# Kernel tuning notes

Measured on AMD Instinct MI355X. Metric: run time of the kernel, lower is better.

## Reference

```python
import jax, jax.numpy as jnp
import numpy as np

SIZE_A, SIZE_B = 5, 5
C, B, H, W = 20, 2, 64, 2048


def _gauss_depthwise_kernel(size_a, size_b, num_classes, sq_var):
    # per-class 2D gaussian with zeroed center; shape (C, 1, ka, kb) for depthwise OIHW
    ii = (np.arange(size_a) - size_a // 2).astype(np.float32)
    jj = (np.arange(size_b) - size_b // 2).astype(np.float32)
    d2 = ii[:, None] ** 2 + jj[None, :] ** 2  # (ka, kb)
    sv = np.asarray(sq_var, dtype=np.float32)[:, None, None]  # (C,1,1)
    k = np.exp(-d2[None] / (2.0 * sv))  # (C, ka, kb)
    k[:, size_a // 2, size_b // 2] = 0.0
    return jnp.asarray(k[:, None], dtype=jnp.float32)


def _depthwise_conv(x, w):
    pa, pb = w.shape[2] // 2, w.shape[3] // 2
    return jax.lax.conv_general_dilated(
        x, w, window_strides=(1, 1), padding=((pa, pa), (pb, pb)),
        dimension_numbers=("NCHW", "OIHW", "NCHW"),
        feature_group_count=x.shape[1])


def setup_inputs() -> dict:
    key = jax.random.key(0)
    k1, k2, k3 = jax.random.split(key, 3)
    sq_var_ang = np.ones(C, dtype=np.float32)
    sq_var_bi = sq_var_ang  # sq_var_bi=None -> defaults to sq_var_ang
    return {
        "data": jax.random.normal(k1, (B, C, H, W), dtype=jnp.float32),
        "mask": jax.random.uniform(k2, (B, 1, H, W), dtype=jnp.float32),
        "bilateral": jax.random.uniform(k3, (B, 1, SIZE_A * SIZE_B - 1, H, W), dtype=jnp.float32),
        "ang_w": _gauss_depthwise_kernel(SIZE_A, SIZE_B, C, sq_var_ang),
        "bi_w": _gauss_depthwise_kernel(SIZE_A, SIZE_B, C, sq_var_bi),
    }


def reference(data, mask, bilateral, ang_w, bi_w):
    b, c, h, w = data.shape
    ka, kb = ang_w.shape[2], ang_w.shape[3]
    pa, pb = ka // 2, kb // 2
    K = ka * kb - 1

    # ang_conv / bi_ang_conv: dense CxC conv whose kernel is diagonal == depthwise gaussian conv
    ang = _depthwise_conv(data, ang_w)
    bi_ang = _depthwise_conv(data, bi_w)

    # condense_conv: one-hot kernels == neighbor extraction of masked data (zero-padded),
    # channel order (neighbor, class) exactly as the torch kernel layout, center removed.
    xm = data * mask
    xp = jnp.pad(xm, ((0, 0), (0, 0), (pa, pa), (pb, pb)))
    neigh = [xp[:, :, i:i + h, j:j + w]
             for i in range(ka) for j in range(kb)
             if not (i == pa and j == pb)]
    cond = jnp.stack(neigh, axis=1)  # (b, K, c, h, w) -- row-major flat order (neighbor, class)
    # torch .view(b, c, -1, h, w) reinterprets the (K*c) channel axis row-major as (c, K):
    cond = cond.reshape(b, c, K, h, w)

    bi_out = (cond * bilateral).sum(axis=2) * mask * bi_ang
    return ang, bi_out
```

## Files before the change

kernel.cpp:

```cpp
#include <hip/hip_runtime.h>

#define C_     20
#define H_     64
#define W_     2048
#define HW_    (H_*W_)
#define KN     24
#define TH     8
#define TW     64
#define TR     (TH+4)
#define TC     (TW+4)
#define PLANE  (TR*TC)
#define DELEMS (C_*PLANE)
#define DPAD   16384
#define NTHR   512
#define DSTG   (DPAD/NTHR)
#define MPAD   1024

#define GLOAD_LDS(SRC, DST)                                                     \
    __builtin_amdgcn_global_load_lds(                                           \
        (const __attribute__((address_space(1))) void*)(SRC),                   \
        (__attribute__((address_space(3))) void*)(DST), 4, 0, 0)

constexpr int KI[KN] = {0,0,0,0,0, 1,1,1,1,1, 2,2,2,2, 3,3,3,3,3, 4,4,4,4,4};
constexpr int KJ[KN] = {0,1,2,3,4, 0,1,2,3,4, 0,1,3,4, 0,1,2,3,4, 0,1,2,3,4};

__global__ __launch_bounds__(NTHR, 4) void lp_kernel(
    const float* __restrict__ data,
    const float* __restrict__ mask,
    const float* __restrict__ bilat,
    const float* __restrict__ ang_w,
    const float* __restrict__ bi_w,
    const float* __restrict__ zbuf,
    float* __restrict__ out)
{
    __shared__ float s_data[DPAD];
    __shared__ float s_mask[MPAD];

    const int tid = threadIdx.x;
    int bid = blockIdx.x;
    bid = (bid & 7)*64 + (bid >> 3);

    const int tx = bid & 31;
    const int ty = (bid >> 5) & 7;
    const int b  = bid >> 8;
    const int y0 = ty*TH, x0 = tx*TW;

    const float* dbase = data + (size_t)b*C_*HW_;
    const float* mbase = mask + (size_t)b*HW_;
    const int wbase = tid & ~63;

#pragma unroll
    for (int s = 0; s < DSTG; ++s) {
        const int idx = tid + s*NTHR;
        const int cls = idx / PLANE;
        const int rem = idx - cls*PLANE;
        const int r   = rem / TC;
        const int col = rem - r*TC;
        const int gy = y0 + r - 2, gx = x0 + col - 2;
        const bool ok = (idx < DELEMS) & (gy >= 0) & (gy < H_) & (gx >= 0) & (gx < W_);
        const float* src = ok ? (dbase + (size_t)cls*HW_ + (gy*W_ + gx)) : zbuf;
        GLOAD_LDS(src, s_data + s*NTHR + wbase);
    }
#pragma unroll
    for (int s = 0; s < MPAD/NTHR; ++s) {
        const int idx = tid + s*NTHR;
        const int r   = idx / TC;
        const int col = idx - r*TC;
        const int gy = y0 + r - 2, gx = x0 + col - 2;
        const bool ok = (idx < PLANE) & (gy >= 0) & (gy < H_) & (gx >= 0) & (gx < W_);
        const float* src = ok ? (mbase + (gy*W_ + gx)) : zbuf;
        GLOAD_LDS(src, s_mask + s*NTHR + wbase);
    }

    const int lx  = tid & 63;
    const int lyy = tid >> 6;
    const int y = y0 + lyy, x = x0 + lx;

    float bb[KN];
    {
        const float* bibase = bilat + (size_t)b*KN*HW_ + (size_t)y*W_ + x;
#pragma unroll
        for (int kp = 0; kp < KN; ++kp) bb[kp] = bibase[(size_t)kp*HW_];
    }

    __syncthreads();

    float mm[KN];
#pragma unroll
    for (int k = 0; k < KN; ++k) mm[k] = s_mask[(lyy + KI[k])*TC + (lx + KJ[k])];
    const float m_c = s_mask[(lyy + 2)*TC + (lx + 2)];

    float bi_acc[C_], biang[C_];
#pragma unroll
    for (int c2 = 0; c2 < C_; ++c2) bi_acc[c2] = 0.0f;

    float* aout = out + ((size_t)b*C_*H_ + y)*W_ + x;
    float* bout = aout + (size_t)2*C_*HW_;

#pragma unroll
    for (int cls = 0; cls < C_; ++cls) {
        float a = 0.0f, ba = 0.0f;
        const float* srow = s_data + cls*PLANE + lyy*TC + lx;
#pragma unroll
        for (int k = 0; k < KN; ++k) {
            const int i = KI[k], j = KJ[k];
            const float v = srow[i*TC + j];
            a  += ang_w[cls*25 + i*5 + j] * v;
            ba += bi_w [cls*25 + i*5 + j] * v;
            const int flat = k*C_ + cls;
            bi_acc[flat / KN] += bb[flat % KN] * (v * mm[k]);
        }
        aout[(size_t)cls*HW_] = a;
        biang[cls] = ba;
    }

#pragma unroll
    for (int c2 = 0; c2 < C_; ++c2)
        bout[(size_t)c2*HW_] = m_c * biang[c2] * bi_acc[c2];
}

extern "C" void kernel_launch(void* const* d_in, const int* in_sizes, int n_in,
                              void* d_out, int out_size, void* d_ws, size_t ws_size,
                              hipStream_t stream) {
    const float* data  = (const float*)d_in[0];
    const float* mask  = (const float*)d_in[1];
    const float* bilat = (const float*)d_in[2];
    const float* ang_w = (const float*)d_in[3];
    const float* bi_w  = (const float*)d_in[4];
    float* out = (float*)d_out;

    hipMemsetAsync(d_ws, 0, 256, stream);

    const int nblocks = 2 * (H_/TH) * (W_/TW);
    lp_kernel<<<nblocks, NTHR, 0, stream>>>(data, mask, bilat, ang_w, bi_w,
                                            (const float*)d_ws, out);
}
```

Before: 33.55 us.

## Transpose shared data tile to class-innermost layout and loop neighbors outermost

The data tile in LDS is stored as position-major with 21-float padded class stride instead of class planes, loaded through registers rather than direct global-to-LDS loads. The compute loop is reordered to iterate neighbors outermost and read all 20 classes contiguously per neighbor, keeping a, ba and bi accumulators in registers. This is meant to cut LDS address computation and enable wider LDS reads. In exchange it raises register pressure (60 accumulators plus 24 bilateral values), and the LDS writes from the strided transpose may bank-conflict.

```diff
diff --git a/kernel.cpp b/kernel.cpp
--- a/kernel.cpp
+++ b/kernel.cpp
@@ -11,9 +11,9 @@
 #define TC     (TW+4)
 #define PLANE  (TR*TC)
 #define DELEMS (C_*PLANE)
-#define DPAD   16384
 #define NTHR   512
-#define DSTG   (DPAD/NTHR)
+#define DSTG   32
+#define SCLS   21
 #define MPAD   1024
 
 #define GLOAD_LDS(SRC, DST)                                                     \
@@ -33,7 +33,7 @@
     const float* __restrict__ zbuf,
     float* __restrict__ out)
 {
-    __shared__ float s_data[DPAD];
+    __shared__ float s_data[PLANE*SCLS];
     __shared__ float s_mask[MPAD];
 
     const int tid = threadIdx.x;
@@ -49,18 +49,17 @@
     const float* mbase = mask + (size_t)b*HW_;
     const int wbase = tid & ~63;
 
+    const int lx  = tid & 63;
+    const int lyy = tid >> 6;
+    const int y = y0 + lyy, x = x0 + lx;
+
+    float bb[KN];
+    {
+        const float* bibase = bilat + (size_t)b*KN*HW_ + (size_t)y*W_ + x;
 #pragma unroll
-    for (int s = 0; s < DSTG; ++s) {
-        const int idx = tid + s*NTHR;
-        const int cls = idx / PLANE;
-        const int rem = idx - cls*PLANE;
-        const int r   = rem / TC;
-        const int col = rem - r*TC;
-        const int gy = y0 + r - 2, gx = x0 + col - 2;
-        const bool ok = (idx < DELEMS) & (gy >= 0) & (gy < H_) & (gx >= 0) & (gx < W_);
-        const float* src = ok ? (dbase + (size_t)cls*HW_ + (gy*W_ + gx)) : zbuf;
-        GLOAD_LDS(src, s_data + s*NTHR + wbase);
+        for (int kp = 0; kp < KN; ++kp) bb[kp] = bibase[(size_t)kp*HW_];
     }
+
 #pragma unroll
     for (int s = 0; s < MPAD/NTHR; ++s) {
         const int idx = tid + s*NTHR;
@@ -72,51 +71,57 @@
         GLOAD_LDS(src, s_mask + s*NTHR + wbase);
     }
 
-    const int lx  = tid & 63;
-    const int lyy = tid >> 6;
-    const int y = y0 + lyy, x = x0 + lx;
+#pragma unroll
+    for (int s = 0; s < DSTG; ++s) {
+        const int g = tid + s*NTHR;
+        if (g < DELEMS) {
+            const int cls = g / PLANE;
+            const int pos = g - cls*PLANE;
+            const int r   = pos / TC;
+            const int col = pos - r*TC;
+            const int gy = y0 + r - 2, gx = x0 + col - 2;
+            const bool ok = (gy >= 0) & (gy < H_) & (gx >= 0) & (gx < W_);
+            const float* src = ok ? (dbase + (size_t)cls*HW_ + (gy*W_ + gx)) : dbase;
+            float v = *src;
+            s_data[pos*SCLS + cls] = ok ? v : 0.0f;
+        }
+    }
+    __syncthreads();
 
-    float bb[KN];
-    {
-        const float* bibase = bilat + (size_t)b*KN*HW_ + (size_t)y*W_ + x;
+    float a[C_], ba[C_], bi[C_];
 #pragma unroll
-        for (int kp = 0; kp < KN; ++kp) bb[kp] = bibase[(size_t)kp*HW_];
+    for (int c = 0; c < C_; ++c) { a[c] = 0.0f; ba[c] = 0.0f; bi[c] = 0.0f; }
+
+    const float* sbase = s_data + (lyy*TC + lx)*SCLS;
+    const int    mbase_l = lyy*TC + lx;
+
+#pragma unroll
+    for (int k = 0; k < KN; ++k) {
+        const int i = KI[k], j = KJ[k];
+        const float mm_k = s_mask[mbase_l + i*TC + j];
+        const float* p = sbase + (i*TC + j)*SCLS;
+        float v[C_];
+#pragma unroll
+        for (int c = 0; c < C_; ++c) v[c] = p[c];
+#pragma unroll
+        for (int c = 0; c < C_; ++c) {
+            a[c]  = fmaf(ang_w[c*25 + i*5 + j], v[c], a[c]);
+            ba[c] = fmaf(bi_w [c*25 + i*5 + j], v[c], ba[c]);
+            const int flat = k*C_ + c;
+            bi[flat/KN] = fmaf(bb[flat%KN], v[c]*mm_k, bi[flat/KN]);
+        }
     }
 
-    __syncthreads();
-
-    float mm[KN];
-#pragma unroll
-    for (int k = 0; k < KN; ++k) mm[k] = s_mask[(lyy + KI[k])*TC + (lx + KJ[k])];
-    const float m_c = s_mask[(lyy + 2)*TC + (lx + 2)];
-
-    float bi_acc[C_], biang[C_];
-#pragma unroll
-    for (int c2 = 0; c2 < C_; ++c2) bi_acc[c2] = 0.0f;
+    const float m_c = s_mask[mbase_l + 2*TC + 2];
 
     float* aout = out + ((size_t)b*C_*H_ + y)*W_ + x;
     float* bout = aout + (size_t)2*C_*HW_;
 
 #pragma unroll
-    for (int cls = 0; cls < C_; ++cls) {
-        float a = 0.0f, ba = 0.0f;
-        const float* srow = s_data + cls*PLANE + lyy*TC + lx;
-#pragma unroll
-        for (int k = 0; k < KN; ++k) {
-            const int i = KI[k], j = KJ[k];
-            const float v = srow[i*TC + j];
-            a  += ang_w[cls*25 + i*5 + j] * v;
-            ba += bi_w [cls*25 + i*5 + j] * v;
-            const int flat = k*C_ + cls;
-            bi_acc[flat / KN] += bb[flat % KN] * (v * mm[k]);
-        }
-        aout[(size_t)cls*HW_] = a;
-        biang[cls] = ba;
+    for (int c = 0; c < C_; ++c) {
+        aout[(size_t)c*HW_] = a[c];
+        bout[(size_t)c*HW_] = m_c * ba[c] * bi[c];
     }
-
-#pragma unroll
-    for (int c2 = 0; c2 < C_; ++c2)
-        bout[(size_t)c2*HW_] = m_c * biang[c2] * bi_acc[c2];
 }
 
 extern "C" void kernel_launch(void* const* d_in, const int* in_sizes, int n_in,
```

Result: slower. 101.3 us (+201.8%).

## Split class staging into two LDS chunks to overlap loads with compute

Applied to the files above, without the earlier changes.

The 20-class data tile is now staged into LDS as two halves of 10 classes in separate buffers. The second half's global-to-LDS loads are issued after the first barrier, so they can run while the first half is being convolved. A second barrier waits for them before the second half is computed. This targets the stall where every thread waits for the whole 20-class tile to arrive before any arithmetic starts, at the cost of one extra block-wide barrier. It also leaves an unused file-scope shared array behind.

```diff
diff --git a/kernel.cpp b/kernel.cpp
--- a/kernel.cpp
+++ b/kernel.cpp
@@ -10,11 +10,11 @@
 #define TR     (TH+4)
 #define TC     (TW+4)
 #define PLANE  (TR*TC)
-#define DELEMS (C_*PLANE)
-#define DPAD   16384
 #define NTHR   512
-#define DSTG   (DPAD/NTHR)
-#define MPAD   1024
+#define NCH    10
+#define CHELE  (NCH*PLANE)
+#define CHPAD  8192
+#define CSTG   (CHPAD/NTHR)
 
 #define GLOAD_LDS(SRC, DST)                                                     \
     __builtin_amdgcn_global_load_lds(                                           \
@@ -23,6 +23,34 @@
 
 constexpr int KI[KN] = {0,0,0,0,0, 1,1,1,1,1, 2,2,2,2, 3,3,3,3,3, 4,4,4,4,4};
 constexpr int KJ[KN] = {0,1,2,3,4, 0,1,2,3,4, 0,1,3,4, 0,1,2,3,4, 0,1,2,3,4};
+
+__shared__ float s_data[2*CHPAD];
+
+template<int CHUNK>
+__device__ __forceinline__ void compute_chunk(
+    const float* __restrict__ sbuf, int lyy, int lx,
+    const float* __restrict__ ang_w, const float* __restrict__ bi_w,
+    const float (&bb)[KN], const float (&mm)[KN],
+    float (&bi)[C_], float (&biang)[C_], float* __restrict__ aout)
+{
+#pragma unroll
+    for (int cl = 0; cl < NCH; ++cl) {
+        const int cls = CHUNK*NCH + cl;
+        float a = 0.0f, ba = 0.0f;
+        const float* srow = sbuf + cl*PLANE + lyy*TC + lx;
+#pragma unroll
+        for (int k = 0; k < KN; ++k) {
+            const int i = KI[k], j = KJ[k];
+            const float v = srow[i*TC + j];
+            a  += ang_w[cls*25 + i*5 + j] * v;
+            ba += bi_w [cls*25 + i*5 + j] * v;
+            const int flat = k*C_ + cls;
+            bi[flat/KN] += bb[flat%KN] * (v * mm[k]);
+        }
+        aout[(size_t)cls*HW_] = a;
+        biang[cls] = ba;
+    }
+}
 
 __global__ __launch_bounds__(NTHR, 4) void lp_kernel(
     const float* __restrict__ data,
@@ -33,8 +61,8 @@
     const float* __restrict__ zbuf,
     float* __restrict__ out)
 {
-    __shared__ float s_data[DPAD];
-    __shared__ float s_mask[MPAD];
+    __shared__ float s_buf[2*CHPAD];
+    __shared__ float s_mask[1024];
 
     const int tid = threadIdx.x;
     int bid = blockIdx.x;
@@ -49,20 +77,26 @@
     const float* mbase = mask + (size_t)b*HW_;
     const int wbase = tid & ~63;
 
+    #define STAGE(CHUNK, BUF) do {                                                   \
+        _Pragma("unroll")                                                            \
+        for (int s = 0; s < CSTG; ++s) {                                             \
+            const int idx = tid + s*NTHR;                                            \
+            const int c   = idx / PLANE;                                             \
+            const int rem = idx - c*PLANE;                                           \
+            const int r   = rem / TC;                                                \
+            const int col = rem - r*TC;                                              \
+            const int gy = y0 + r - 2, gx = x0 + col - 2;                            \
+            const bool ok = (idx < CHELE) & (gy >= 0) & (gy < H_) &                  \
+                            (gx >= 0) & (gx < W_);                                   \
+            const float* src = ok                                                    \
+                ? (dbase + (size_t)((CHUNK)*NCH + c)*HW_ + (gy*W_ + gx)) : zbuf;     \
+            GLOAD_LDS(src, s_buf + (BUF)*CHPAD + s*NTHR + wbase);                    \
+        }                                                                            \
+    } while (0)
+
+    STAGE(0, 0);
 #pragma unroll
-    for (int s = 0; s < DSTG; ++s) {
-        const int idx = tid + s*NTHR;
-        const int cls = idx / PLANE;
-        const int rem = idx - cls*PLANE;
-        const int r   = rem / TC;
-        const int col = rem - r*TC;
-        const int gy = y0 + r - 2, gx = x0 + col - 2;
-        const bool ok = (idx < DELEMS) & (gy >= 0) & (gy < H_) & (gx >= 0) & (gx < W_);
-        const float* src = ok ? (dbase + (size_t)cls*HW_ + (gy*W_ + gx)) : zbuf;
-        GLOAD_LDS(src, s_data + s*NTHR + wbase);
-    }
-#pragma unroll
-    for (int s = 0; s < MPAD/NTHR; ++s) {
+    for (int s = 0; s < 2; ++s) {
         const int idx = tid + s*NTHR;
         const int r   = idx / TC;
         const int col = idx - r*TC;
@@ -85,38 +119,31 @@
 
     __syncthreads();
 
+    STAGE(1, 1);
+
     float mm[KN];
 #pragma unroll
     for (int k = 0; k < KN; ++k) mm[k] = s_mask[(lyy + KI[k])*TC + (lx + KJ[k])];
     const float m_c = s_mask[(lyy + 2)*TC + (lx + 2)];
 
-    float bi_acc[C_], biang[C_];
+    float bi[C_], biang[C_];
 #pragma unroll
-    for (int c2 = 0; c2 < C_; ++c2) bi_acc[c2] = 0.0f;
+    for (int c = 0; c < C_; ++c) { bi[c] = 0.0f; }
 
     float* aout = out + ((size_t)b*C_*H_ + y)*W_ + x;
     float* bout = aout + (size_t)2*C_*HW_;
 
-#pragma unroll
-    for (int cls = 0; cls < C_; ++cls) {
-        float a = 0.0f, ba = 0.0f;
-        const float* srow = s_data + cls*PLANE + lyy*TC + lx;
-#pragma unroll
-        for (int k = 0; k < KN; ++k) {
-            const int i = KI[k], j = KJ[k];
-            const float v = srow[i*TC + j];
-            a  += ang_w[cls*25 + i*5 + j] * v;
-            ba += bi_w [cls*25 + i*5 + j] * v;
-            const int flat = k*C_ + cls;
-            bi_acc[flat / KN] += bb[flat % KN] * (v * mm[k]);
-        }
-        aout[(size_t)cls*HW_] = a;
-        biang[cls] = ba;
-    }
+    compute_chunk<0>(s_buf,         lyy, lx, ang_w, bi_w, bb, mm, bi, biang, aout);
+
+    __syncthreads();
+
+    compute_chunk<1>(s_buf + CHPAD, lyy, lx, ang_w, bi_w, bb, mm, bi, biang, aout);
 
 #pragma unroll
-    for (int c2 = 0; c2 < C_; ++c2)
-        bout[(size_t)c2*HW_] = m_c * biang[c2] * bi_acc[c2];
+    for (int c = 0; c < C_; ++c)
+        bout[(size_t)c*HW_] = m_c * biang[c] * bi[c];
+
+    #undef STAGE
 }
 
 extern "C" void kernel_launch(void* const* d_in, const int* in_sizes, int n_in,
```

Result: no change. 33.81 us (+0.8%).

## Stream bilateral weights in class groups and spill bi_ang through output buffer

Applied to the files above, without the earlier changes.

Reorders the class loop into four residue groups so each group needs only 6 of the 24 bilateral weights live in registers, loaded just before use rather than all up front. The per-class bi_ang values are written to the output buffer as m_c*ba and later read back and multiplied by the accumulated bilateral sum, instead of being held in a 20-entry register array. It also drops the occupancy hint from launch_bounds. The aim is lower register pressure, at the cost of an extra global write and read round trip per output and less early latency hiding for the bilateral loads.

```diff
diff --git a/kernel.cpp b/kernel.cpp
--- a/kernel.cpp
+++ b/kernel.cpp
@@ -13,8 +13,7 @@
 #define DELEMS (C_*PLANE)
 #define DPAD   16384
 #define NTHR   512
-#define DSTG   (DPAD/NTHR)
-#define MPAD   1024
+#define DSTG   32
 
 #define GLOAD_LDS(SRC, DST)                                                     \
     __builtin_amdgcn_global_load_lds(                                           \
@@ -24,7 +23,7 @@
 constexpr int KI[KN] = {0,0,0,0,0, 1,1,1,1,1, 2,2,2,2, 3,3,3,3,3, 4,4,4,4,4};
 constexpr int KJ[KN] = {0,1,2,3,4, 0,1,2,3,4, 0,1,3,4, 0,1,2,3,4, 0,1,2,3,4};
 
-__global__ __launch_bounds__(NTHR, 4) void lp_kernel(
+__global__ __launch_bounds__(NTHR) void lp_kernel(
     const float* __restrict__ data,
     const float* __restrict__ mask,
     const float* __restrict__ bilat,
@@ -34,7 +33,7 @@
     float* __restrict__ out)
 {
     __shared__ float s_data[DPAD];
-    __shared__ float s_mask[MPAD];
+    __shared__ float s_mask[1024];
 
     const int tid = threadIdx.x;
     int bid = blockIdx.x;
@@ -62,7 +61,7 @@
         GLOAD_LDS(src, s_data + s*NTHR + wbase);
     }
 #pragma unroll
-    for (int s = 0; s < MPAD/NTHR; ++s) {
+    for (int s = 0; s < 2; ++s) {
         const int idx = tid + s*NTHR;
         const int r   = idx / TC;
         const int col = idx - r*TC;
@@ -76,13 +75,6 @@
     const int lyy = tid >> 6;
     const int y = y0 + lyy, x = x0 + lx;
 
-    float bb[KN];
-    {
-        const float* bibase = bilat + (size_t)b*KN*HW_ + (size_t)y*W_ + x;
-#pragma unroll
-        for (int kp = 0; kp < KN; ++kp) bb[kp] = bibase[(size_t)kp*HW_];
-    }
-
     __syncthreads();
 
     float mm[KN];
@@ -90,33 +82,47 @@
     for (int k = 0; k < KN; ++k) mm[k] = s_mask[(lyy + KI[k])*TC + (lx + KJ[k])];
     const float m_c = s_mask[(lyy + 2)*TC + (lx + 2)];
 
-    float bi_acc[C_], biang[C_];
+    float bi[C_];
 #pragma unroll
-    for (int c2 = 0; c2 < C_; ++c2) bi_acc[c2] = 0.0f;
+    for (int c = 0; c < C_; ++c) bi[c] = 0.0f;
 
     float* aout = out + ((size_t)b*C_*H_ + y)*W_ + x;
     float* bout = aout + (size_t)2*C_*HW_;
+    const float* bibase = bilat + (size_t)b*KN*HW_ + (size_t)y*W_ + x;
 
 #pragma unroll
-    for (int cls = 0; cls < C_; ++cls) {
-        float a = 0.0f, ba = 0.0f;
-        const float* srow = s_data + cls*PLANE + lyy*TC + lx;
+    for (int rg = 0; rg < 4; ++rg) {
+        float bbsub[6];
 #pragma unroll
-        for (int k = 0; k < KN; ++k) {
-            const int i = KI[k], j = KJ[k];
-            const float v = srow[i*TC + j];
-            a  += ang_w[cls*25 + i*5 + j] * v;
-            ba += bi_w [cls*25 + i*5 + j] * v;
-            const int flat = k*C_ + cls;
-            bi_acc[flat / KN] += bb[flat % KN] * (v * mm[k]);
+        for (int u = 0; u < 6; ++u)
+            bbsub[u] = bibase[(size_t)(rg + 4*u)*HW_];
+
+#pragma unroll
+        for (int t = 0; t < 5; ++t) {
+            const int cls = rg + 4*t;
+            float a = 0.0f, ba = 0.0f;
+            const float* srow = s_data + cls*PLANE + lyy*TC + lx;
+#pragma unroll
+            for (int k = 0; k < KN; ++k) {
+                const int i = KI[k], j = KJ[k];
+                const float v = srow[i*TC + j];
+                a  += ang_w[cls*25 + i*5 + j] * v;
+                ba += bi_w [cls*25 + i*5 + j] * v;
+                const int flat = k*C_ + cls;
+                const int jj   = flat % KN;
+                bi[flat / KN] += bbsub[(jj - rg) / 4] * (v * mm[k]);
+            }
+            aout[(size_t)cls*HW_] = a;
+            bout[(size_t)cls*HW_] = m_c * ba;
         }
-        aout[(size_t)cls*HW_] = a;
-        biang[cls] = ba;
     }
 
+    asm volatile("s_waitcnt vmcnt(0)" ::: "memory");
 #pragma unroll
-    for (int c2 = 0; c2 < C_; ++c2)
-        bout[(size_t)c2*HW_] = m_c * biang[c2] * bi_acc[c2];
+    for (int c = 0; c < C_; ++c) {
+        float p = bout[(size_t)c*HW_];
+        bout[(size_t)c*HW_] = p * bi[c];
+    }
 }
 
 extern "C" void kernel_launch(void* const* d_in, const int* in_sizes, int n_in,
```

Measured after the change: 45.11 us. 34.4% more time.
